# Kernel tuning notes

Measured on AMD Instinct MI355X. Metric: run time of the kernel, lower is better.

The kernel has to match this reference:

```python
import jax, jax.numpy as jnp
import numpy as np

G, K, P = 200000, 32, 2048
TOP_K = 5
MIN_DIST = 0.1
EPS = 1e-8


def setup_inputs() -> dict:
    key = jax.random.key(0)
    k1, k2, k3, k4, k5 = jax.random.split(key, 5)
    A_logits = jax.random.normal(k1, (G, K), dtype=jnp.float32) * 0.01
    x = jax.random.normal(k2, (G, 3), dtype=jnp.float32)
    weights = jax.random.uniform(k3, (G,), dtype=jnp.float32)
    # scale so pred_mask = sum_g R[p,g] ~ 0.5 (rows of softmax(A) sum to 1)
    R = jax.random.uniform(k4, (P, G), dtype=jnp.float32) * (1.0 / G)
    instance_mask = jax.random.randint(k5, (P,), 0, 2, dtype=jnp.int32)
    return {"A_logits": A_logits, "x": x, "weights": weights, "R": R,
            "instance_mask": instance_mask}


def _total_loss(A_logits, x, weights, R, instance_mask):
    A = jax.nn.softmax(A_logits, axis=1)  # (G, K)

    # --- render mask loss (BCE on clamped soft mask) ---
    r_pc = R @ A                                   # (P, K)
    pred = jnp.clip(r_pc.sum(axis=1), 0.0, 1.0)    # (P,)
    t = instance_mask.astype(jnp.float32)
    log_p = jnp.maximum(jnp.log(pred), -100.0)     # torch BCE clamps log at -100
    log_1mp = jnp.maximum(jnp.log1p(-pred), -100.0)
    render = -jnp.mean(t * log_p + (1.0 - t) * log_1mp)

    # --- cluster stats + dispersion loss ---
    Aw = A * weights[:, None]                      # (G, K)
    occupancy = Aw.sum(axis=0) + EPS               # (K,)
    centroids = (Aw.T @ x) / occupancy[:, None]    # (K, 3)
    diff = x[None, :, :] - centroids[:, None, :]   # (K, G, 3)
    sq_dist = (diff ** 2).sum(-1)                  # (K, G)
    dispersion = (sq_dist * Aw.T).sum(axis=1) / occupancy  # (K,)
    disp = dispersion.sum()

    # --- separation loss: sum_{i<j} relu(min_dist - ||c_i - c_j||)^2 ---
    d = jnp.linalg.norm(centroids[:, None, :] - centroids[None, :, :], axis=-1)  # (K, K)
    pen = jax.nn.relu(MIN_DIST - d) ** 2
    sep = jnp.sum(jnp.triu(pen, k=1))

    # --- covisibility loss: per-gaussian pairwise sq-diffs of top-k probs ---
    # sum_{i<j} (v_i - v_j)^2 = k * sum v_i^2 - (sum v_i)^2
    top_vals, _ = jax.lax.top_k(A, TOP_K)          # (G, TOP_K)
    pair = TOP_K * (top_vals ** 2).sum(axis=1) - top_vals.sum(axis=1) ** 2
    cov = pair.mean()

    # --- prune loss ---
    prune = jnp.abs(weights).sum()

    return render + disp + sep + cov + prune


def reference(A_logits, x, weights, R, instance_mask):
    return _total_loss(A_logits, x, weights, R, instance_mask)
```

## Files before the change

kernel.cpp:

```cpp
#include <hip/hip_runtime.h>

#define G_N 200000
#define K_N 32
#define P_N 2048
#define EPSV 1e-8f
#define MINDIST 0.1f

#define PA_BLOCKS ((G_N + 255) / 256)
#define TOTAL_BLOCKS (PA_BLOCKS + P_N)

__device__ __forceinline__ float wave_reduce_sum(float v) {
#pragma unroll
  for (int d = 1; d < 64; d <<= 1) v += __shfl_xor(v, d, 64);
  return v;
}

__global__ __launch_bounds__(256) void fused_main(
    const float* __restrict__ A, const float* __restrict__ x,
    const float* __restrict__ wts, const float* __restrict__ R,
    float* __restrict__ pred_sum, float* __restrict__ acc)
{
  __shared__ float smem[164];
  const int tid  = threadIdx.x;
  const int lane = tid & 63;
  const int wid  = tid >> 6;

  if (blockIdx.x >= PA_BLOCKS) {
    const int p = blockIdx.x - PA_BLOCKS;
    const float4* row = (const float4*)(R + (size_t)p * G_N);
    float s0 = 0.f, s1 = 0.f;
    int i = tid;
    for (; i + 256 < (G_N / 4); i += 512) {
      float4 v0 = row[i];
      float4 v1 = row[i + 256];
      s0 += (v0.x + v0.y) + (v0.z + v0.w);
      s1 += (v1.x + v1.y) + (v1.z + v1.w);
    }
    for (; i < (G_N / 4); i += 256) {
      float4 v = row[i];
      s0 += (v.x + v.y) + (v.z + v.w);
    }
    float s = wave_reduce_sum(s0 + s1);
    if (lane == 0) smem[wid] = s;
    __syncthreads();
    if (tid == 0) pred_sum[p] = (smem[0] + smem[1]) + (smem[2] + smem[3]);
    return;
  }

  const int g = blockIdx.x * 256 + tid;
  for (int i = tid; i < 162; i += 256) smem[i] = 0.f;
  __syncthreads();

  float p[K_N];
  float covp = 0.f, prw = 0.f;
  float wg = 0.f, x0 = 0.f, x1 = 0.f, x2 = 0.f, q = 0.f;

  if (g < G_N) {
    const float4* Ar = (const float4*)(A + (size_t)g * K_N);
    float a[K_N];
#pragma unroll
    for (int j = 0; j < 8; j++) {
      float4 v = Ar[j];
      a[4 * j + 0] = v.x; a[4 * j + 1] = v.y;
      a[4 * j + 2] = v.z; a[4 * j + 3] = v.w;
    }
    float m = a[0];
#pragma unroll
    for (int k = 1; k < K_N; k++) m = fmaxf(m, a[k]);
    float s = 0.f;
#pragma unroll
    for (int k = 0; k < K_N; k++) { p[k] = __expf(a[k] - m); s += p[k]; }
    const float invs = 1.f / s;

    float t0 = 0.f, t1 = 0.f, t2 = 0.f, t3 = 0.f, t4 = 0.f;
#pragma unroll
    for (int k = 0; k < K_N; k++) {
      p[k] *= invs;
      float v = p[k], mx;
      mx = fmaxf(t0, v); v = fminf(t0, v); t0 = mx;
      mx = fmaxf(t1, v); v = fminf(t1, v); t1 = mx;
      mx = fmaxf(t2, v); v = fminf(t2, v); t2 = mx;
      mx = fmaxf(t3, v); v = fminf(t3, v); t3 = mx;
      mx = fmaxf(t4, v); v = fminf(t4, v); t4 = mx;
    }
    float d01 = t0 - t1, d02 = t0 - t2, d03 = t0 - t3, d04 = t0 - t4;
    float d12 = t1 - t2, d13 = t1 - t3, d14 = t1 - t4;
    float d23 = t2 - t3, d24 = t2 - t4, d34 = t3 - t4;
    covp = d01*d01 + d02*d02 + d03*d03 + d04*d04 + d12*d12
         + d13*d13 + d14*d14 + d23*d23 + d24*d24 + d34*d34;

    wg = wts[g];
    prw = fabsf(wg);
    x0 = x[3 * g + 0]; x1 = x[3 * g + 1]; x2 = x[3 * g + 2];
    q = x0 * x0 + x1 * x1 + x2 * x2;
  } else {
#pragma unroll
    for (int k = 0; k < K_N; k++) p[k] = 0.f;
  }

#pragma unroll
  for (int k = 0; k < K_N; k++) {
    float c = wg * p[k];
    float v0 = c, v1 = c * x0, v2 = c * x1, v3 = c * x2, v4 = c * q;
#pragma unroll
    for (int d = 1; d < 64; d <<= 1) {
      v0 += __shfl_xor(v0, d, 64);
      v1 += __shfl_xor(v1, d, 64);
      v2 += __shfl_xor(v2, d, 64);
      v3 += __shfl_xor(v3, d, 64);
      v4 += __shfl_xor(v4, d, 64);
    }
    if (lane == 0) {
      atomicAdd(&smem[k],       v0);
      atomicAdd(&smem[32 + k],  v1);
      atomicAdd(&smem[64 + k],  v2);
      atomicAdd(&smem[96 + k],  v3);
      atomicAdd(&smem[128 + k], v4);
    }
  }
  covp = wave_reduce_sum(covp);
  prw  = wave_reduce_sum(prw);
  if (lane == 0) {
    atomicAdd(&smem[160], covp);
    atomicAdd(&smem[161], prw);
  }
  __syncthreads();
  if (tid < 162) atomicAdd(&acc[tid], smem[tid]);
}

__global__ __launch_bounds__(256) void finalize_k(
    const float* __restrict__ pred_sum, const int* __restrict__ mask,
    const float* __restrict__ acc, float* __restrict__ out)
{
  __shared__ float sred[4];
  __shared__ float cent[K_N][3];
  const int tid  = threadIdx.x;
  const int lane = tid & 63;
  const int wid  = tid >> 6;

  float bce = 0.f;
  for (int i = tid; i < P_N; i += 256) {
    float pred = fminf(fmaxf(pred_sum[i], 0.f), 1.f);
    float t = (float)mask[i];
    float lp = fmaxf(logf(pred), -100.f);
    float l1 = fmaxf(log1pf(-pred), -100.f);
    bce += t * lp + (1.f - t) * l1;
  }
  bce = wave_reduce_sum(bce);
  if (lane == 0) sred[wid] = bce;
  __syncthreads();
  const float render = -((sred[0] + sred[1]) + (sred[2] + sred[3])) / (float)P_N;

  float disp_v = 0.f, sep_v = 0.f;
  if (tid < K_N) {
    float W  = acc[tid];
    float Sx = acc[32 + tid], Sy = acc[64 + tid], Sz = acc[96 + tid];
    float Q  = acc[128 + tid];
    float occ = W + EPSV;
    float inv = 1.f / occ;
    float cx = Sx * inv, cy = Sy * inv, cz = Sz * inv;
    cent[tid][0] = cx; cent[tid][1] = cy; cent[tid][2] = cz;
    disp_v = (Q - 2.f * (cx * Sx + cy * Sy + cz * Sz)
              + (cx * cx + cy * cy + cz * cz) * W) * inv;
  }
  __syncthreads();

  if (tid < K_N) {
    for (int j = tid + 1; j < K_N; j++) {
      float dx = cent[tid][0] - cent[j][0];
      float dy = cent[tid][1] - cent[j][1];
      float dz = cent[tid][2] - cent[j][2];
      float d = sqrtf(dx * dx + dy * dy + dz * dz);
      float r = fmaxf(MINDIST - d, 0.f);
      sep_v += r * r;
    }
  }
  if (tid < 64) {
    float dsum = wave_reduce_sum(disp_v);
    float ssum = wave_reduce_sum(sep_v);
    if (tid == 0) {
      float cov   = acc[160] / (float)G_N;
      float prune = acc[161];
      out[0] = render + dsum + ssum + cov + prune;
    }
  }
}

extern "C" void kernel_launch(void* const* d_in, const int* in_sizes, int n_in,
                              void* d_out, int out_size, void* d_ws, size_t ws_size,
                              hipStream_t stream) {
  const float* A    = (const float*)d_in[0];
  const float* x    = (const float*)d_in[1];
  const float* wts  = (const float*)d_in[2];
  const float* R    = (const float*)d_in[3];
  const int*   mask = (const int*)d_in[4];
  float* out = (float*)d_out;

  float* ws       = (float*)d_ws;
  float* pred_sum = ws;
  float* acc      = ws + P_N;

  hipMemsetAsync(acc, 0, 162 * sizeof(float), stream);
  fused_main<<<TOTAL_BLOCKS, 256, 0, stream>>>(A, x, wts, R, pred_sum, acc);
  finalize_k<<<1, 256, 0, stream>>>(pred_sum, mask, acc, out);
}
```

Baseline: 310.0 us.

## Split R row sums into four chunks per row with nontemporal loads

Each row of R is now summed by four blocks instead of one, and the partial sums are combined with atomicAdd into pred_sum, which is zeroed by the widened memset. R blocks now come first in the grid, and the R stream uses nontemporal loads so it bypasses cache retention. The aim is more parallelism and shorter per-block tails when streaming the large R matrix, at the cost of more blocks and global atomics.

```diff
diff --git a/kernel.cpp b/kernel.cpp
--- a/kernel.cpp
+++ b/kernel.cpp
@@ -6,8 +6,13 @@
 #define EPSV 1e-8f
 #define MINDIST 0.1f
 
+#define CHUNKS_PER_ROW 4
+#define CHUNK_F4 ((G_N / 4) / CHUNKS_PER_ROW)
+#define N_RCHUNKS (P_N * CHUNKS_PER_ROW)
 #define PA_BLOCKS ((G_N + 255) / 256)
-#define TOTAL_BLOCKS (PA_BLOCKS + P_N)
+#define TOTAL_BLOCKS (N_RCHUNKS + PA_BLOCKS)
+
+typedef float f4v __attribute__((ext_vector_type(4)));
 
 __device__ __forceinline__ float wave_reduce_sum(float v) {
 #pragma unroll
@@ -25,29 +30,31 @@
   const int lane = tid & 63;
   const int wid  = tid >> 6;
 
-  if (blockIdx.x >= PA_BLOCKS) {
-    const int p = blockIdx.x - PA_BLOCKS;
-    const float4* row = (const float4*)(R + (size_t)p * G_N);
+  if (blockIdx.x < N_RCHUNKS) {
+    const int c    = blockIdx.x;
+    const int row  = c >> 2;
+    const int part = c & 3;
+    const f4v* ch = (const f4v*)(R + (size_t)row * G_N) + (size_t)part * CHUNK_F4;
     float s0 = 0.f, s1 = 0.f;
     int i = tid;
-    for (; i + 256 < (G_N / 4); i += 512) {
-      float4 v0 = row[i];
-      float4 v1 = row[i + 256];
+    for (; i + 256 < CHUNK_F4; i += 512) {
+      f4v v0 = __builtin_nontemporal_load(&ch[i]);
+      f4v v1 = __builtin_nontemporal_load(&ch[i + 256]);
       s0 += (v0.x + v0.y) + (v0.z + v0.w);
       s1 += (v1.x + v1.y) + (v1.z + v1.w);
     }
-    for (; i < (G_N / 4); i += 256) {
-      float4 v = row[i];
+    for (; i < CHUNK_F4; i += 256) {
+      f4v v = __builtin_nontemporal_load(&ch[i]);
       s0 += (v.x + v.y) + (v.z + v.w);
     }
     float s = wave_reduce_sum(s0 + s1);
     if (lane == 0) smem[wid] = s;
     __syncthreads();
-    if (tid == 0) pred_sum[p] = (smem[0] + smem[1]) + (smem[2] + smem[3]);
+    if (tid == 0) atomicAdd(&pred_sum[row], (smem[0] + smem[1]) + (smem[2] + smem[3]));
     return;
   }
 
-  const int g = blockIdx.x * 256 + tid;
+  const int g = (blockIdx.x - N_RCHUNKS) * 256 + tid;
   for (int i = tid; i < 162; i += 256) smem[i] = 0.f;
   __syncthreads();
 
@@ -200,7 +207,7 @@
   float* pred_sum = ws;
   float* acc      = ws + P_N;
 
-  hipMemsetAsync(acc, 0, 162 * sizeof(float), stream);
+  hipMemsetAsync(ws, 0, (P_N + 162) * sizeof(float), stream);
   fused_main<<<TOTAL_BLOCKS, 256, 0, stream>>>(A, x, wts, R, pred_sum, acc);
   finalize_k<<<1, 256, 0, stream>>>(pred_sum, mask, acc, out);
 }
```

After: 320.4 us. 3.3% more time.

## Transpose per-gaussian cluster weights through LDS to cut shuffle reductions

Applied to the files above, without the earlier changes.

Each thread writes its weighted softmax row and its position/squared-norm into shared memory. Threads are then regrouped so each sums 8 gaussians for 4 clusters, followed by a 3-step shuffle reduction instead of 32×5 full 6-step wave reductions. The change also folds the softmax normalisation into the weight scaling and unrolls the R row-sum loop four ways. It costs about 38KB of LDS per block, which may reduce occupancy for the R-streaming blocks that share this kernel.

```diff
diff --git a/kernel.cpp b/kernel.cpp
--- a/kernel.cpp
+++ b/kernel.cpp
@@ -7,7 +7,8 @@
 #define MINDIST 0.1f
 
 #define PA_BLOCKS ((G_N + 255) / 256)
-#define TOTAL_BLOCKS (PA_BLOCKS + P_N)
+#define TOTAL_BLOCKS (P_N + PA_BLOCKS)
+#define PW_S 36
 
 __device__ __forceinline__ float wave_reduce_sum(float v) {
 #pragma unroll
@@ -21,6 +22,8 @@
     float* __restrict__ pred_sum, float* __restrict__ acc)
 {
   __shared__ float smem[164];
+  __shared__ float pw[256 * PW_S];
+  __shared__ float4 xq[256];
   const int tid  = threadIdx.x;
   const int lane = tid & 63;
   const int wid  = tid >> 6;
@@ -28,19 +31,23 @@
   if (blockIdx.x >= PA_BLOCKS) {
     const int p = blockIdx.x - PA_BLOCKS;
     const float4* row = (const float4*)(R + (size_t)p * G_N);
-    float s0 = 0.f, s1 = 0.f;
+    float s0 = 0.f, s1 = 0.f, s2 = 0.f, s3 = 0.f;
     int i = tid;
-    for (; i + 256 < (G_N / 4); i += 512) {
+    for (; i + 768 < (G_N / 4); i += 1024) {
       float4 v0 = row[i];
       float4 v1 = row[i + 256];
+      float4 v2 = row[i + 512];
+      float4 v3 = row[i + 768];
       s0 += (v0.x + v0.y) + (v0.z + v0.w);
       s1 += (v1.x + v1.y) + (v1.z + v1.w);
+      s2 += (v2.x + v2.y) + (v2.z + v2.w);
+      s3 += (v3.x + v3.y) + (v3.z + v3.w);
     }
     for (; i < (G_N / 4); i += 256) {
       float4 v = row[i];
       s0 += (v.x + v.y) + (v.z + v.w);
     }
-    float s = wave_reduce_sum(s0 + s1);
+    float s = wave_reduce_sum((s0 + s1) + (s2 + s3));
     if (lane == 0) smem[wid] = s;
     __syncthreads();
     if (tid == 0) pred_sum[p] = (smem[0] + smem[1]) + (smem[2] + smem[3]);
@@ -48,76 +55,107 @@
   }
 
   const int g = blockIdx.x * 256 + tid;
-  for (int i = tid; i < 162; i += 256) smem[i] = 0.f;
-  __syncthreads();
-
-  float p[K_N];
+  if (tid < 164) smem[tid] = 0.f;
+
+  float av[K_N];
   float covp = 0.f, prw = 0.f;
-  float wg = 0.f, x0 = 0.f, x1 = 0.f, x2 = 0.f, q = 0.f;
+  float4 xv = make_float4(0.f, 0.f, 0.f, 0.f);
 
   if (g < G_N) {
     const float4* Ar = (const float4*)(A + (size_t)g * K_N);
-    float a[K_N];
 #pragma unroll
     for (int j = 0; j < 8; j++) {
       float4 v = Ar[j];
-      a[4 * j + 0] = v.x; a[4 * j + 1] = v.y;
-      a[4 * j + 2] = v.z; a[4 * j + 3] = v.w;
-    }
-    float m = a[0];
-#pragma unroll
-    for (int k = 1; k < K_N; k++) m = fmaxf(m, a[k]);
+      av[4 * j + 0] = v.x; av[4 * j + 1] = v.y;
+      av[4 * j + 2] = v.z; av[4 * j + 3] = v.w;
+    }
+    float m = av[0];
+#pragma unroll
+    for (int k = 1; k < K_N; k++) m = fmaxf(m, av[k]);
     float s = 0.f;
 #pragma unroll
-    for (int k = 0; k < K_N; k++) { p[k] = __expf(a[k] - m); s += p[k]; }
+    for (int k = 0; k < K_N; k++) { av[k] = __expf(av[k] - m); s += av[k]; }
     const float invs = 1.f / s;
 
     float t0 = 0.f, t1 = 0.f, t2 = 0.f, t3 = 0.f, t4 = 0.f;
 #pragma unroll
     for (int k = 0; k < K_N; k++) {
-      p[k] *= invs;
-      float v = p[k], mx;
+      float v = av[k], mx;
       mx = fmaxf(t0, v); v = fminf(t0, v); t0 = mx;
       mx = fmaxf(t1, v); v = fminf(t1, v); t1 = mx;
       mx = fmaxf(t2, v); v = fminf(t2, v); t2 = mx;
       mx = fmaxf(t3, v); v = fminf(t3, v); t3 = mx;
       mx = fmaxf(t4, v); v = fminf(t4, v); t4 = mx;
     }
+    t0 *= invs; t1 *= invs; t2 *= invs; t3 *= invs; t4 *= invs;
     float d01 = t0 - t1, d02 = t0 - t2, d03 = t0 - t3, d04 = t0 - t4;
     float d12 = t1 - t2, d13 = t1 - t3, d14 = t1 - t4;
     float d23 = t2 - t3, d24 = t2 - t4, d34 = t3 - t4;
     covp = d01*d01 + d02*d02 + d03*d03 + d04*d04 + d12*d12
          + d13*d13 + d14*d14 + d23*d23 + d24*d24 + d34*d34;
 
-    wg = wts[g];
+    const float wg = wts[g];
     prw = fabsf(wg);
-    x0 = x[3 * g + 0]; x1 = x[3 * g + 1]; x2 = x[3 * g + 2];
-    q = x0 * x0 + x1 * x1 + x2 * x2;
+    const float x0 = x[3 * g + 0], x1 = x[3 * g + 1], x2 = x[3 * g + 2];
+    xv = make_float4(x0, x1, x2, x0 * x0 + x1 * x1 + x2 * x2);
+
+    const float cw = wg * invs;
+#pragma unroll
+    for (int k = 0; k < K_N; k++) av[k] *= cw;
   } else {
 #pragma unroll
-    for (int k = 0; k < K_N; k++) p[k] = 0.f;
-  }
-
-#pragma unroll
-  for (int k = 0; k < K_N; k++) {
-    float c = wg * p[k];
-    float v0 = c, v1 = c * x0, v2 = c * x1, v3 = c * x2, v4 = c * q;
-#pragma unroll
-    for (int d = 1; d < 64; d <<= 1) {
-      v0 += __shfl_xor(v0, d, 64);
-      v1 += __shfl_xor(v1, d, 64);
-      v2 += __shfl_xor(v2, d, 64);
-      v3 += __shfl_xor(v3, d, 64);
-      v4 += __shfl_xor(v4, d, 64);
-    }
-    if (lane == 0) {
-      atomicAdd(&smem[k],       v0);
-      atomicAdd(&smem[32 + k],  v1);
-      atomicAdd(&smem[64 + k],  v2);
-      atomicAdd(&smem[96 + k],  v3);
-      atomicAdd(&smem[128 + k], v4);
-    }
-  }
+    for (int k = 0; k < K_N; k++) av[k] = 0.f;
+  }
+
+#pragma unroll
+  for (int j = 0; j < 8; j++)
+    *(float4*)&pw[tid * PW_S + 4 * j] =
+        make_float4(av[4*j+0], av[4*j+1], av[4*j+2], av[4*j+3]);
+  xq[tid] = xv;
+  __syncthreads();
+
+  const int kq  = tid & 7;
+  const int sub = tid >> 3;
+  float4 aW = make_float4(0,0,0,0), aX = aW, aY = aW, aZ = aW, aQ = aW;
+#pragma unroll
+  for (int i = 0; i < 8; i++) {
+    const int gg = sub * 8 + i;
+    const float4 cv = *(const float4*)&pw[gg * PW_S + kq * 4];
+    const float4 xg = xq[gg];
+    aW.x += cv.x;        aW.y += cv.y;        aW.z += cv.z;        aW.w += cv.w;
+    aX.x += cv.x * xg.x; aX.y += cv.y * xg.x; aX.z += cv.z * xg.x; aX.w += cv.w * xg.x;
+    aY.x += cv.x * xg.y; aY.y += cv.y * xg.y; aY.z += cv.z * xg.y; aY.w += cv.w * xg.y;
+    aZ.x += cv.x * xg.z; aZ.y += cv.y * xg.z; aZ.z += cv.z * xg.z; aZ.w += cv.w * xg.z;
+    aQ.x += cv.x * xg.w; aQ.y += cv.y * xg.w; aQ.z += cv.z * xg.w; aQ.w += cv.w * xg.w;
+  }
+
+#pragma unroll
+  for (int d = 8; d <= 32; d <<= 1) {
+    aW.x += __shfl_xor(aW.x, d, 64); aW.y += __shfl_xor(aW.y, d, 64);
+    aW.z += __shfl_xor(aW.z, d, 64); aW.w += __shfl_xor(aW.w, d, 64);
+    aX.x += __shfl_xor(aX.x, d, 64); aX.y += __shfl_xor(aX.y, d, 64);
+    aX.z += __shfl_xor(aX.z, d, 64); aX.w += __shfl_xor(aX.w, d, 64);
+    aY.x += __shfl_xor(aY.x, d, 64); aY.y += __shfl_xor(aY.y, d, 64);
+    aY.z += __shfl_xor(aY.z, d, 64); aY.w += __shfl_xor(aY.w, d, 64);
+    aZ.x += __shfl_xor(aZ.x, d, 64); aZ.y += __shfl_xor(aZ.y, d, 64);
+    aZ.z += __shfl_xor(aZ.z, d, 64); aZ.w += __shfl_xor(aZ.w, d, 64);
+    aQ.x += __shfl_xor(aQ.x, d, 64); aQ.y += __shfl_xor(aQ.y, d, 64);
+    aQ.z += __shfl_xor(aQ.z, d, 64); aQ.w += __shfl_xor(aQ.w, d, 64);
+  }
+  if (lane < 8) {
+    const int k0 = lane * 4;
+    atomicAdd(&smem[      k0+0], aW.x); atomicAdd(&smem[      k0+1], aW.y);
+    atomicAdd(&smem[      k0+2], aW.z); atomicAdd(&smem[      k0+3], aW.w);
+    atomicAdd(&smem[ 32 + k0+0], aX.x); atomicAdd(&smem[ 32 + k0+1], aX.y);
+    atomicAdd(&smem[ 32 + k0+2], aX.z); atomicAdd(&smem[ 32 + k0+3], aX.w);
+    atomicAdd(&smem[ 64 + k0+0], aY.x); atomicAdd(&smem[ 64 + k0+1], aY.y);
+    atomicAdd(&smem[ 64 + k0+2], aY.z); atomicAdd(&smem[ 64 + k0+3], aY.w);
+    atomicAdd(&smem[ 96 + k0+0], aZ.x); atomicAdd(&smem[ 96 + k0+1], aZ.y);
+    atomicAdd(&smem[ 96 + k0+2], aZ.z); atomicAdd(&smem[ 96 + k0+3], aZ.w);
+    atomicAdd(&smem[128 + k0+0], aQ.x); atomicAdd(&smem[128 + k0+1], aQ.y);
+    atomicAdd(&smem[128 + k0+2], aQ.z); atomicAdd(&smem[128 + k0+3], aQ.w);
+  }
+
   covp = wave_reduce_sum(covp);
   prw  = wave_reduce_sum(prw);
   if (lane == 0) {
```

Measured after the change: 317.3 us. 2.3% more time.
